# Kernel optimization log

Hardware: AMD Instinct MI355X
Metric: run time of the kernel (lower is better)

Reference implementation:

```python
import jax, jax.numpy as jnp
import numpy as np

EPS = 1e-05


def setup_inputs() -> dict:
    key = jax.random.key(0)
    ks = jax.random.split(key, 6)
    B, L, D = 16, 4096, 1024
    x = jax.random.normal(ks[0], (B, L, D), dtype=jnp.float32)
    prev_count = jax.random.randint(ks[1], (B,), 1, 5).astype(jnp.int32)  # prior_count-like, >=1
    prev_mean = jnp.zeros((B, D), dtype=jnp.float32)   # prior_mean init = 0
    prev_var = jnp.ones((B, D), dtype=jnp.float32)     # exp(prior_logv) with logv init 0
    weight = 0.02 * jax.random.normal(ks[2], (D,), dtype=jnp.float32)
    bias = 0.02 * jax.random.normal(ks[3], (D,), dtype=jnp.float32)
    padding_mask = jax.random.randint(ks[4], (B, L), 0, 2).astype(bool)  # True = padded
    return {"x": x, "prev_count": prev_count, "prev_mean": prev_mean,
            "prev_var": prev_var, "weight": weight, "bias": bias,
            "padding_mask": padding_mask}


def _timestep_norm(x, prev_count, prev_mean, prev_var, gamma, beta, padding_mask, eps):
    # x: [B, L, D]; Welford running mean/var over timesteps, skipping padded steps.
    B, L, D = x.shape
    valid = (~padding_mask).astype(x.dtype)          # [B, L], 1 = valid step
    x_t = jnp.swapaxes(x, 0, 1)                      # [L, B, D]
    m_t = valid.T                                    # [L, B]

    def step(carry, inp):
        count, mean, var = carry                     # [B], [B,D], [B,D]
        xt, m = inp                                  # [B,D], [B]
        mb = m[:, None]                              # [B,1]
        new_count = count + m                        # [B]
        denom = jnp.maximum(new_count, 1.0)[:, None]
        delta = xt - mean
        new_mean = mean + mb * delta / denom
        var_upd = (count[:, None] * var + delta * (xt - new_mean)) / denom
        new_var = jnp.where(mb > 0, var_upd, var)
        y = (gamma * (xt - new_mean) * jax.lax.rsqrt(new_var + eps) + beta) * mb
        return (new_count, new_mean, new_var), y

    init = (prev_count.astype(x.dtype), prev_mean, prev_var)
    (count, mean, var), ys = jax.lax.scan(step, init, (x_t, m_t))
    y = jnp.swapaxes(ys, 0, 1)                       # [B, L, D]
    return y, count, mean, var


def reference(x, prev_count, prev_mean, prev_var, weight, bias, padding_mask):
    gamma = weight + 1.0
    return _timestep_norm(x, prev_count, prev_mean, prev_var, gamma, bias,
                          padding_mask, EPS)
```

## Files before the change

kernel.cpp:

```cpp
#include <hip/hip_runtime.h>


#define Bn 16
#define Ln 4096
#define Dn 1024
#define D4 (Dn / 4)
#define Cn 64
#define CLn (Ln / Cn)
#define EPSf 1e-5f

__global__ __launch_bounds__(256) void tn_chunk_stats(
    const float* __restrict__ x, const int* __restrict__ mask,
    float4* __restrict__ mean_ws, float4* __restrict__ m2_ws,
    float* __restrict__ cnt_ws)
{
    int idx = blockIdx.x * 256 + threadIdx.x;
    int d4 = idx & (D4 - 1);
    int bc = idx >> 8;
    int c  = bc & (Cn - 1);
    int b  = bc >> 6;

    const float4* xp = (const float4*)(x + ((size_t)b * Ln + (size_t)c * CLn) * Dn) + d4;
    const int*    mp = mask + b * Ln + c * CLn;

    float n = 0.f;
    float4 mean = {0.f, 0.f, 0.f, 0.f};
    float4 M2   = {0.f, 0.f, 0.f, 0.f};
    #pragma unroll 8
    for (int i = 0; i < CLn; ++i) {
        float4 xv = xp[(size_t)i * D4];
        if (mp[i] == 0) {
            n += 1.f;
            float rn = 1.f / n;
            float dx, dy, dz, dw;
            dx = xv.x - mean.x; mean.x += dx * rn; M2.x += dx * (xv.x - mean.x);
            dy = xv.y - mean.y; mean.y += dy * rn; M2.y += dy * (xv.y - mean.y);
            dz = xv.z - mean.z; mean.z += dz * rn; M2.z += dz * (xv.z - mean.z);
            dw = xv.w - mean.w; mean.w += dw * rn; M2.w += dw * (xv.w - mean.w);
        }
    }
    mean_ws[idx] = mean;
    m2_ws[idx]   = M2;
    if (d4 == 0) cnt_ws[bc] = n;
}

__global__ __launch_bounds__(256) void tn_scan(
    const int* __restrict__ prev_count, const float4* __restrict__ prev_mean,
    const float4* __restrict__ prev_var,
    float4* __restrict__ mean_ws, float4* __restrict__ m2_ws,
    const float* __restrict__ cnt_ws, float* __restrict__ cnt_pref,
    float* __restrict__ out_count, float4* __restrict__ out_mean,
    float4* __restrict__ out_var)
{
    int idx = blockIdx.x * 256 + threadIdx.x;
    int d4 = idx & (D4 - 1);
    int b  = idx >> 8;

    float  n    = (float)prev_count[b];
    float4 mean = prev_mean[idx];
    float4 var  = prev_var[idx];
    float4 M2   = {var.x * n, var.y * n, var.z * n, var.w * n};

    #pragma unroll 4
    for (int c = 0; c < Cn; ++c) {
        int rc = b * Cn + c;
        int o  = rc * D4 + d4;
        float  nc  = cnt_ws[rc];
        float4 mc  = mean_ws[o];
        float4 m2c = m2_ws[o];
        mean_ws[o] = mean;
        m2_ws[o]   = M2;
        if (d4 == 0) cnt_pref[rc] = n;
        float nn = n + nc;
        float wB = nc / nn;
        float s  = n * wB;
        float dx = mc.x - mean.x, dy = mc.y - mean.y,
              dz = mc.z - mean.z, dw = mc.w - mean.w;
        mean.x += dx * wB; mean.y += dy * wB;
        mean.z += dz * wB; mean.w += dw * wB;
        M2.x += m2c.x + dx * dx * s; M2.y += m2c.y + dy * dy * s;
        M2.z += m2c.z + dz * dz * s; M2.w += m2c.w + dw * dw * s;
        n = nn;
    }
    out_mean[idx] = mean;
    float rn = 1.f / n;
    out_var[idx] = {M2.x * rn, M2.y * rn, M2.z * rn, M2.w * rn};
    if (d4 == 0) out_count[b] = n;
}

__global__ __launch_bounds__(256) void tn_emit(
    const float* __restrict__ x, const int* __restrict__ mask,
    const float* __restrict__ weight, const float* __restrict__ bias,
    const float4* __restrict__ mean_ws, const float4* __restrict__ m2_ws,
    const float* __restrict__ cnt_pref, float* __restrict__ y)
{
    int idx = blockIdx.x * 256 + threadIdx.x;
    int d4 = idx & (D4 - 1);
    int bc = idx >> 8;
    int c  = bc & (Cn - 1);
    int b  = bc >> 6;

    size_t base = ((size_t)b * Ln + (size_t)c * CLn) * Dn;
    const float4* xp = (const float4*)(x + base) + d4;
    float4*       yp = (float4*)(y + base) + d4;
    const int*    mp = mask + b * Ln + c * CLn;

    float  n    = cnt_pref[bc];
    float4 mean = mean_ws[idx];
    float4 M2   = m2_ws[idx];
    const float4 w4 = ((const float4*)weight)[d4];
    const float4 b4 = ((const float4*)bias)[d4];
    float gx = w4.x + 1.f, gy = w4.y + 1.f, gz = w4.z + 1.f, gw = w4.w + 1.f;

    #pragma unroll 4
    for (int i = 0; i < CLn; ++i) {
        float4 yv = {0.f, 0.f, 0.f, 0.f};
        if (mp[i] == 0) {
            float4 xv = xp[(size_t)i * D4];
            n += 1.f;
            float rn = 1.f / n;
            float dx, d2;
            dx = xv.x - mean.x; mean.x += dx * rn; d2 = xv.x - mean.x;
            M2.x += dx * d2; yv.x = gx * d2 * rsqrtf(M2.x * rn + EPSf) + b4.x;
            dx = xv.y - mean.y; mean.y += dx * rn; d2 = xv.y - mean.y;
            M2.y += dx * d2; yv.y = gy * d2 * rsqrtf(M2.y * rn + EPSf) + b4.y;
            dx = xv.z - mean.z; mean.z += dx * rn; d2 = xv.z - mean.z;
            M2.z += dx * d2; yv.z = gz * d2 * rsqrtf(M2.z * rn + EPSf) + b4.z;
            dx = xv.w - mean.w; mean.w += dx * rn; d2 = xv.w - mean.w;
            M2.w += dx * d2; yv.w = gw * d2 * rsqrtf(M2.w * rn + EPSf) + b4.w;
        }
        yp[(size_t)i * D4] = yv;
    }
}

extern "C" void kernel_launch(void* const* d_in, const int* in_sizes, int n_in,
                              void* d_out, int out_size, void* d_ws, size_t ws_size,
                              hipStream_t stream)
{
    const float* x          = (const float*)d_in[0];
    const int*   prev_count = (const int*)d_in[1];
    const float* prev_mean  = (const float*)d_in[2];
    const float* prev_var   = (const float*)d_in[3];
    const float* weight     = (const float*)d_in[4];
    const float* bias       = (const float*)d_in[5];
    const int*   mask       = (const int*)d_in[6];

    float* y         = (float*)d_out;
    float* out_count = y + (size_t)Bn * Ln * Dn;
    float* out_mean  = out_count + Bn;
    float* out_var   = out_mean + (size_t)Bn * Dn;

    float* mean_ws  = (float*)d_ws;
    float* m2_ws    = mean_ws + (size_t)Bn * Cn * Dn;
    float* cnt_ws   = m2_ws + (size_t)Bn * Cn * Dn;
    float* cnt_pref = cnt_ws + Bn * Cn;

    tn_chunk_stats<<<(Bn * Cn * D4) / 256, 256, 0, stream>>>(
        x, mask, (float4*)mean_ws, (float4*)m2_ws, cnt_ws);
    tn_scan<<<(Bn * D4) / 256, 256, 0, stream>>>(
        prev_count, (const float4*)prev_mean, (const float4*)prev_var,
        (float4*)mean_ws, (float4*)m2_ws, cnt_ws, cnt_pref,
        out_count, (float4*)out_mean, (float4*)out_var);
    tn_emit<<<(Bn * Cn * D4) / 256, 256, 0, stream>>>(
        x, mask, weight, bias, (const float4*)mean_ws, (const float4*)m2_ws,
        cnt_pref, y);
}
```

Before: 510.9 us.

## Parallelize chunk-combine scan across wavefront lanes and double chunk count

Replaces the serial per-thread scan over chunks with a wavefront-wide parallel prefix scan using shuffles and Chan's merge formula, with each lane handling two chunks. The workspace layout is transposed so each (batch, feature-quad) owns a contiguous run of chunk stats. The chunk count rises from 64 to 128, which shortens the sequential loops in the stats and emit kernels and increases the number of threads. The cost is more workspace traffic, more register pressure from shuffling nine floats per step, and strided workspace writes from the stats and emit kernels.

```diff
diff --git a/kernel.cpp b/kernel.cpp
--- a/kernel.cpp
+++ b/kernel.cpp
@@ -5,9 +5,35 @@
 #define Ln 4096
 #define Dn 1024
 #define D4 (Dn / 4)
-#define Cn 64
+#define Cn 128
 #define CLn (Ln / Cn)
 #define EPSf 1e-5f
+
+struct St { float n; float4 m; float4 s; };
+
+__device__ __forceinline__ St chan_merge(const St& A, const St& B) {
+    St R;
+    R.n = A.n + B.n;
+    float wB = B.n / fmaxf(R.n, 1.f);
+    float sc = A.n * wB;
+    float dx = B.m.x - A.m.x, dy = B.m.y - A.m.y,
+          dz = B.m.z - A.m.z, dw = B.m.w - A.m.w;
+    R.m.x = A.m.x + dx * wB; R.m.y = A.m.y + dy * wB;
+    R.m.z = A.m.z + dz * wB; R.m.w = A.m.w + dw * wB;
+    R.s.x = A.s.x + B.s.x + dx * dx * sc; R.s.y = A.s.y + B.s.y + dy * dy * sc;
+    R.s.z = A.s.z + B.s.z + dz * dz * sc; R.s.w = A.s.w + B.s.w + dw * dw * sc;
+    return R;
+}
+
+__device__ __forceinline__ St shfl_up_st(const St& v, int delta) {
+    St r;
+    r.n   = __shfl_up(v.n,   delta, 64);
+    r.m.x = __shfl_up(v.m.x, delta, 64); r.m.y = __shfl_up(v.m.y, delta, 64);
+    r.m.z = __shfl_up(v.m.z, delta, 64); r.m.w = __shfl_up(v.m.w, delta, 64);
+    r.s.x = __shfl_up(v.s.x, delta, 64); r.s.y = __shfl_up(v.s.y, delta, 64);
+    r.s.z = __shfl_up(v.s.z, delta, 64); r.s.w = __shfl_up(v.s.w, delta, 64);
+    return r;
+}
 
 __global__ __launch_bounds__(256) void tn_chunk_stats(
     const float* __restrict__ x, const int* __restrict__ mask,
@@ -18,7 +44,7 @@
     int d4 = idx & (D4 - 1);
     int bc = idx >> 8;
     int c  = bc & (Cn - 1);
-    int b  = bc >> 6;
+    int b  = bc >> 7;
 
     const float4* xp = (const float4*)(x + ((size_t)b * Ln + (size_t)c * CLn) * Dn) + d4;
     const int*    mp = mask + b * Ln + c * CLn;
@@ -32,15 +58,16 @@
         if (mp[i] == 0) {
             n += 1.f;
             float rn = 1.f / n;
-            float dx, dy, dz, dw;
+            float dx;
             dx = xv.x - mean.x; mean.x += dx * rn; M2.x += dx * (xv.x - mean.x);
-            dy = xv.y - mean.y; mean.y += dy * rn; M2.y += dy * (xv.y - mean.y);
-            dz = xv.z - mean.z; mean.z += dz * rn; M2.z += dz * (xv.z - mean.z);
-            dw = xv.w - mean.w; mean.w += dw * rn; M2.w += dw * (xv.w - mean.w);
+            dx = xv.y - mean.y; mean.y += dx * rn; M2.y += dx * (xv.y - mean.y);
+            dx = xv.z - mean.z; mean.z += dx * rn; M2.z += dx * (xv.z - mean.z);
+            dx = xv.w - mean.w; mean.w += dx * rn; M2.w += dx * (xv.w - mean.w);
         }
     }
-    mean_ws[idx] = mean;
-    m2_ws[idx]   = M2;
+    int o = (b * D4 + d4) * Cn + c;
+    mean_ws[o] = mean;
+    m2_ws[o]   = M2;
     if (d4 == 0) cnt_ws[bc] = n;
 }
 
@@ -52,40 +79,54 @@
     float* __restrict__ out_count, float4* __restrict__ out_mean,
     float4* __restrict__ out_var)
 {
-    int idx = blockIdx.x * 256 + threadIdx.x;
-    int d4 = idx & (D4 - 1);
-    int b  = idx >> 8;
-
-    float  n    = (float)prev_count[b];
-    float4 mean = prev_mean[idx];
-    float4 var  = prev_var[idx];
-    float4 M2   = {var.x * n, var.y * n, var.z * n, var.w * n};
-
-    #pragma unroll 4
-    for (int c = 0; c < Cn; ++c) {
-        int rc = b * Cn + c;
-        int o  = rc * D4 + d4;
-        float  nc  = cnt_ws[rc];
-        float4 mc  = mean_ws[o];
-        float4 m2c = m2_ws[o];
-        mean_ws[o] = mean;
-        m2_ws[o]   = M2;
-        if (d4 == 0) cnt_pref[rc] = n;
-        float nn = n + nc;
-        float wB = nc / nn;
-        float s  = n * wB;
-        float dx = mc.x - mean.x, dy = mc.y - mean.y,
-              dz = mc.z - mean.z, dw = mc.w - mean.w;
-        mean.x += dx * wB; mean.y += dy * wB;
-        mean.z += dz * wB; mean.w += dw * wB;
-        M2.x += m2c.x + dx * dx * s; M2.y += m2c.y + dy * dy * s;
-        M2.z += m2c.z + dz * dz * s; M2.w += m2c.w + dw * dw * s;
-        n = nn;
-    }
-    out_mean[idx] = mean;
-    float rn = 1.f / n;
-    out_var[idx] = {M2.x * rn, M2.y * rn, M2.z * rn, M2.w * rn};
-    if (d4 == 0) out_count[b] = n;
+    int wv   = (blockIdx.x * 256 + threadIdx.x) >> 6;
+    int lane = threadIdx.x & 63;
+    int b  = wv >> 8;
+    int d4 = wv & (D4 - 1);
+    int base = (b * D4 + d4) * Cn;
+    int c0 = 2 * lane, c1 = 2 * lane + 1;
+
+    St s0, s1;
+    s0.n = cnt_ws[b * Cn + c0]; s0.m = mean_ws[base + c0]; s0.s = m2_ws[base + c0];
+    s1.n = cnt_ws[b * Cn + c1]; s1.m = mean_ws[base + c1]; s1.s = m2_ws[base + c1];
+
+    St incl = chan_merge(s0, s1);
+    #pragma unroll
+    for (int off = 1; off < 64; off <<= 1) {
+        St t = shfl_up_st(incl, off);
+        if (lane >= off) incl = chan_merge(t, incl);
+    }
+    St epp = shfl_up_st(incl, 1);
+    if (lane == 0) {
+        epp.n = 0.f;
+        epp.m = {0.f, 0.f, 0.f, 0.f};
+        epp.s = {0.f, 0.f, 0.f, 0.f};
+    }
+
+    float np = (float)prev_count[b];
+    St P;
+    P.n = np;
+    P.m = prev_mean[b * D4 + d4];
+    float4 vp = prev_var[b * D4 + d4];
+    P.s = {vp.x * np, vp.y * np, vp.z * np, vp.w * np};
+
+    St pref0 = chan_merge(P, epp);
+    St pref1 = chan_merge(pref0, s0);
+
+    mean_ws[base + c0] = pref0.m; m2_ws[base + c0] = pref0.s;
+    mean_ws[base + c1] = pref1.m; m2_ws[base + c1] = pref1.s;
+    if (d4 == 0) {
+        cnt_pref[b * Cn + c0] = pref0.n;
+        cnt_pref[b * Cn + c1] = pref1.n;
+    }
+
+    if (lane == 63) {
+        St tot = chan_merge(P, incl);
+        out_mean[b * D4 + d4] = tot.m;
+        float rn = 1.f / tot.n;
+        out_var[b * D4 + d4] = {tot.s.x * rn, tot.s.y * rn, tot.s.z * rn, tot.s.w * rn};
+        if (d4 == 0) out_count[b] = tot.n;
+    }
 }
 
 __global__ __launch_bounds__(256) void tn_emit(
@@ -98,16 +139,17 @@
     int d4 = idx & (D4 - 1);
     int bc = idx >> 8;
     int c  = bc & (Cn - 1);
-    int b  = bc >> 6;
-
-    size_t base = ((size_t)b * Ln + (size_t)c * CLn) * Dn;
-    const float4* xp = (const float4*)(x + base) + d4;
-    float4*       yp = (float4*)(y + base) + d4;
+    int b  = bc >> 7;
+
+    size_t gbase = ((size_t)b * Ln + (size_t)c * CLn) * Dn;
+    const float4* xp = (const float4*)(x + gbase) + d4;
+    float4*       yp = (float4*)(y + gbase) + d4;
     const int*    mp = mask + b * Ln + c * CLn;
 
+    int o = (b * D4 + d4) * Cn + c;
     float  n    = cnt_pref[bc];
-    float4 mean = mean_ws[idx];
-    float4 M2   = m2_ws[idx];
+    float4 mean = mean_ws[o];
+    float4 M2   = m2_ws[o];
     const float4 w4 = ((const float4*)weight)[d4];
     const float4 b4 = ((const float4*)bias)[d4];
     float gx = w4.x + 1.f, gy = w4.y + 1.f, gz = w4.z + 1.f, gw = w4.w + 1.f;
@@ -150,18 +192,17 @@
     float* out_mean  = out_count + Bn;
     float* out_var   = out_mean + (size_t)Bn * Dn;
 
-    float* mean_ws  = (float*)d_ws;
-    float* m2_ws    = mean_ws + (size_t)Bn * Cn * Dn;
-    float* cnt_ws   = m2_ws + (size_t)Bn * Cn * Dn;
-    float* cnt_pref = cnt_ws + Bn * Cn;
+    float4* mean_ws  = (float4*)d_ws;
+    float4* m2_ws    = mean_ws + (size_t)Bn * D4 * Cn;
+    float*  cnt_ws   = (float*)(m2_ws + (size_t)Bn * D4 * Cn);
+    float*  cnt_pref = cnt_ws + Bn * Cn;
 
     tn_chunk_stats<<<(Bn * Cn * D4) / 256, 256, 0, stream>>>(
-        x, mask, (float4*)mean_ws, (float4*)m2_ws, cnt_ws);
-    tn_scan<<<(Bn * D4) / 256, 256, 0, stream>>>(
+        x, mask, mean_ws, m2_ws, cnt_ws);
+    tn_scan<<<(Bn * D4 * 64) / 256, 256, 0, stream>>>(
         prev_count, (const float4*)prev_mean, (const float4*)prev_var,
-        (float4*)mean_ws, (float4*)m2_ws, cnt_ws, cnt_pref,
+        mean_ws, m2_ws, cnt_ws, cnt_pref,
         out_count, (float4*)out_mean, (float4*)out_var);
     tn_emit<<<(Bn * Cn * D4) / 256, 256, 0, stream>>>(
-        x, mask, weight, bias, (const float4*)mean_ws, (const float4*)m2_ws,
-        cnt_pref, y);
-}
+        x, mask, weight, bias, mean_ws, m2_ws, cnt_pref, y);
+}
```

Measured after the change: 502.2 us. Within noise of the previous version (-1.7%).
